# Kernel tuning notes

Measured on AMD Instinct MI355X. Metric: run time of the kernel, lower is better.

The kernel has to match this reference:

```python
import jax, jax.numpy as jnp
import numpy as np

N_NODES = 1536
IN_FEATURES = 1433
N_HIDDEN = 64      # total across 8 heads -> 8 per head
N_HEADS = 8
N_CLASSES = 7
NEG_SLOPE = 0.2    # LeakyReLU slope in GATv2 layer


def setup_inputs() -> dict:
    key = jax.random.key(0)
    k_x, k_adj, k_w1, k_a1, k_w2, k_a2 = jax.random.split(key, 6)
    x = jax.random.normal(k_x, (N_NODES, IN_FEATURES), dtype=jnp.float32)
    adj = jax.random.uniform(k_adj, (N_NODES, N_NODES)) < 0.01
    adj = adj | jnp.eye(N_NODES, dtype=bool)
    adj_mat = adj[:, :, None]  # [n, n, 1]
    # layer 1 (share_weights=True -> one linear for l and r), attn vector shared across heads
    s1 = 1.0 / np.sqrt(IN_FEATURES)
    W1 = jax.random.uniform(k_w1, (IN_FEATURES, N_HIDDEN), minval=-s1, maxval=s1, dtype=jnp.float32)
    a1 = jax.random.uniform(k_a1, (N_HIDDEN // N_HEADS,), minval=-1.0, maxval=1.0, dtype=jnp.float32)
    # layer 2: 1 head, n_classes features, is_concat=False (mean over the single head)
    s2 = 1.0 / np.sqrt(N_HIDDEN)
    W2 = jax.random.uniform(k_w2, (N_HIDDEN, N_CLASSES), minval=-s2, maxval=s2, dtype=jnp.float32)
    a2 = jax.random.uniform(k_a2, (N_CLASSES,), minval=-1.0, maxval=1.0, dtype=jnp.float32)
    return {"x": x, "adj_mat": adj_mat, "W1": W1, "a1": a1, "W2": W2, "a2": a2}


def _gatv2_layer(h, adj, W, a, n_heads, is_concat):
    n = h.shape[0]
    g = (h @ W).reshape(n, n_heads, -1)              # shared weights: g_l == g_r == g
    # pairwise scores: e[i,j,h] = a . leaky_relu(g[j] + g[i])  (symmetric since weights shared)
    s = jax.nn.leaky_relu(g[:, None] + g[None, :], NEG_SLOPE)   # [n, n, heads, f]
    e = jnp.einsum('ijhf,f->ijh', s, a)                          # [n, n, heads]
    e = jnp.where(adj, e, -jnp.inf)                              # adj broadcasts [n,n,1]
    att = jax.nn.softmax(e, axis=1)                              # softmax over source nodes j
    out = jnp.einsum('ijh,jhf->ihf', att, g)                     # [n, heads, f]
    if is_concat:
        return out.reshape(n, -1)
    return out.mean(axis=1)


def reference(x, adj_mat, W1, a1, W2, a2):
    # dropout layers are identity in eval mode
    h = _gatv2_layer(x, adj_mat, W1, a1, N_HEADS, True)   # [n, n_hidden]
    h = jax.nn.elu(h)
    return _gatv2_layer(h, adj_mat, W2, a2, 1, False)     # [n, n_classes]
```

## Files before the change

### kernel.cpp

```cpp
#include <hip/hip_runtime.h>

#define N_NODES 1536
#define IN_F    1433
#define HID     64
#define NH      8
#define HF      8
#define NC      7
#define MAXN    64
#define GST     66
#define G1_BLOCKS 384
#define ROWS    4
#define KQ      92
#define XS2     1472
#define RED_ST  260

__device__ __forceinline__ float waveAllMax(float v) {
#pragma unroll
    for (int o = 32; o > 0; o >>= 1) v = fmaxf(v, __shfl_xor(v, o, 64));
    return v;
}
__device__ __forceinline__ float waveAllSum(float v) {
#pragma unroll
    for (int o = 32; o > 0; o >>= 1) v += __shfl_xor(v, o, 64);
    return v;
}

__global__ __launch_bounds__(256) void k_front(const float* __restrict__ x,
                                               const float* __restrict__ W1,
                                               const unsigned int* __restrict__ adj,
                                               float* __restrict__ g1,
                                               int* __restrict__ cnt,
                                               int* __restrict__ nbr) {
    __shared__ float xs[ROWS * XS2];
    __shared__ float red[16 * RED_ST];
    __shared__ int lc;
    const int t = threadIdx.x;

    if (blockIdx.x < G1_BLOCKS) {
        const int i0 = blockIdx.x * ROWS;
        for (int r = 0; r < ROWS; ++r) {
            const float* xr = x + (size_t)(i0 + r) * IN_F;
            for (int k = t; k < XS2; k += 256)
                xs[r * XS2 + k] = (k < IN_F) ? xr[k] : 0.f;
        }
        __syncthreads();

        const int tc = t & 15;
        const int tq = t >> 4;
        const int k0 = tq * KQ;
        float acc[ROWS][4];
#pragma unroll
        for (int r = 0; r < ROWS; ++r)
#pragma unroll
            for (int cc = 0; cc < 4; ++cc) acc[r][cc] = 0.f;

        for (int kb = k0; kb < k0 + KQ; kb += 4) {
            float wv[4][4];
#pragma unroll
            for (int u = 0; u < 4; ++u) {
                int kc = kb + u;
                if (kc > IN_F - 1) kc = IN_F - 1;
                float4 wq = *(const float4*)(W1 + (size_t)kc * HID + tc * 4);
                wv[u][0] = wq.x; wv[u][1] = wq.y; wv[u][2] = wq.z; wv[u][3] = wq.w;
            }
#pragma unroll
            for (int r = 0; r < ROWS; ++r) {
                float4 xq = *(const float4*)(xs + r * XS2 + kb);
                float xr4[4] = {xq.x, xq.y, xq.z, xq.w};
#pragma unroll
                for (int u = 0; u < 4; ++u)
#pragma unroll
                    for (int cc = 0; cc < 4; ++cc)
                        acc[r][cc] += xr4[u] * wv[u][cc];
            }
        }
#pragma unroll
        for (int r = 0; r < ROWS; ++r)
#pragma unroll
            for (int cc = 0; cc < 4; ++cc)
                red[tq * RED_ST + r * 64 + tc * 4 + cc] = acc[r][cc];
        __syncthreads();
        float s = 0.f;
#pragma unroll
        for (int q = 0; q < 16; ++q) s += red[q * RED_ST + t];
        g1[(size_t)(i0 + (t >> 6)) * HID + (t & 63)] = s;
    } else {
        const int i = blockIdx.x - G1_BLOCKS;
        if (t == 0) lc = 0;
        __syncthreads();
        const unsigned int* row = adj + (size_t)i * N_NODES;
        for (int j = t; j < N_NODES; j += 256) {
            if (row[j] != 0u) {
                int p = atomicAdd(&lc, 1);
                if (p < MAXN) nbr[i * MAXN + p] = j;
            }
        }
        __syncthreads();
        if (t == 0) {
            int n = (lc > MAXN) ? MAXN : lc;
            if (n == 0) { nbr[i * MAXN] = i; n = 1; }
            cnt[i] = n;
        }
    }
}

__global__ __launch_bounds__(128) void k_attn1(const float* __restrict__ g1,
                                               const int* __restrict__ cnt,
                                               const int* __restrict__ nbr,
                                               const float* __restrict__ a1,
                                               const float* __restrict__ W2,
                                               float* __restrict__ g2) {
    __shared__ float gis[HID];
    __shared__ float gj[MAXN * GST];
    __shared__ float es[NH * GST];
    __shared__ float hrow[HID];
    const int i = blockIdx.x, tid = threadIdx.x;
    const int t = tid & 63, w = tid >> 6;
    const int n = cnt[i];

    if (tid < HID) gis[tid] = g1[(size_t)i * HID + tid];
    const int jn = nbr[i * MAXN + t];

    for (int l0 = 4 * w; l0 < n; l0 += 8) {
        float v[4];
#pragma unroll
        for (int u = 0; u < 4; ++u) {
            int l = l0 + u;
            int lc = (l < n) ? l : (n - 1);
            int j = __shfl(jn, lc, 64);
            v[u] = g1[(size_t)j * HID + t];
        }
#pragma unroll
        for (int u = 0; u < 4; ++u)
            if (l0 + u < n) gj[(l0 + u) * GST + t] = v[u];
    }
    __syncthreads();

    float av[HF];
#pragma unroll
    for (int f = 0; f < HF; ++f) av[f] = a1[f];

    float sc[4];
    if (t < n) {
#pragma unroll
        for (int hh = 0; hh < 4; ++hh) {
            const int h = 4 * w + hh;
            float s = 0.f;
#pragma unroll
            for (int f = 0; f < HF; ++f) {
                float v = gis[h * HF + f] + gj[t * GST + h * HF + f];
                v = (v >= 0.f) ? v : 0.2f * v;
                s += av[f] * v;
            }
            sc[hh] = s;
        }
    } else {
#pragma unroll
        for (int hh = 0; hh < 4; ++hh) sc[hh] = -INFINITY;
    }

#pragma unroll
    for (int hh = 0; hh < 4; ++hh) {
        const int h = 4 * w + hh;
        float m = waveAllMax(sc[hh]);
        float p = (t < n) ? __expf(sc[hh] - m) : 0.f;
        float S = waveAllSum(p);
        es[h * GST + t] = p / S;
    }

    const int c = 32 * w + (t & 31);
    const int h = c >> 3;
    float acc = 0.f;
    for (int l = (t >> 5); l < n; l += 2)
        acc += es[h * GST + l] * gj[l * GST + c];
    acc += __shfl_xor(acc, 32, 64);
    float hv = (acc > 0.f) ? acc : (__expf(acc) - 1.f);
    if (t < 32) hrow[c] = hv;
    __syncthreads();

    const float hvt = hrow[t];
#pragma unroll
    for (int cc = 0; cc < 4; ++cc) {
        const int cG = 4 * w + cc;
        if (cG < NC) {
            float v = hvt * W2[t * NC + cG];
            v = waveAllSum(v);
            if (t == 0) g2[(size_t)i * 8 + cG] = v;
        }
    }
}

__global__ __launch_bounds__(64) void k_back(const float* __restrict__ g2,
                                             const float* __restrict__ a2,
                                             const int* __restrict__ cnt,
                                             const int* __restrict__ nbr,
                                             float* __restrict__ out) {
    __shared__ float g2s[MAXN * 8];
    const int i = blockIdx.x, t = threadIdx.x;
    const int n = cnt[i];
    const int jn = nbr[i * MAXN + t];
    const int j = (t < n) ? jn : i;

    float4 lo = *(const float4*)(g2 + (size_t)j * 8);
    float4 hi = *(const float4*)(g2 + (size_t)j * 8 + 4);
    float4 slo = *(const float4*)(g2 + (size_t)i * 8);
    float4 shi = *(const float4*)(g2 + (size_t)i * 8 + 4);
    *(float4*)(g2s + t * 8) = lo;
    *(float4*)(g2s + t * 8 + 4) = hi;
    __syncthreads();

    const float self[NC] = {slo.x, slo.y, slo.z, slo.w, shi.x, shi.y, shi.z};

    float scv;
    if (t < n) {
        float s = 0.f;
#pragma unroll
        for (int c = 0; c < NC; ++c) {
            float v = self[c] + g2s[t * 8 + c];
            v = (v >= 0.f) ? v : 0.2f * v;
            s += a2[c] * v;
        }
        scv = s;
    } else scv = -INFINITY;

    float m = waveAllMax(scv);
    float p = (t < n) ? __expf(scv - m) : 0.f;
    float S = waveAllSum(p);

#pragma unroll
    for (int c = 0; c < NC; ++c) {
        float v = (t < n) ? p * g2s[t * 8 + c] : 0.f;
        float s = waveAllSum(v);
        if (t == c) out[(size_t)i * NC + c] = s / S;
    }
}

extern "C" void kernel_launch(void* const* d_in, const int* in_sizes, int n_in,
                              void* d_out, int out_size, void* d_ws, size_t ws_size,
                              hipStream_t stream) {
    (void)out_size; (void)ws_size;
    const void* px = nullptr; const void* padj = nullptr;
    const void* pW1 = nullptr; const void* pa1 = nullptr;
    const void* pW2 = nullptr; const void* pa2 = nullptr;
    for (int i = 0; i < n_in; ++i) {
        switch (in_sizes[i]) {
            case N_NODES * IN_F:    px   = d_in[i]; break;
            case N_NODES * N_NODES: padj = d_in[i]; break;
            case IN_F * HID:        pW1  = d_in[i]; break;
            case HF:                pa1  = d_in[i]; break;
            case HID * NC:          pW2  = d_in[i]; break;
            case NC:                pa2  = d_in[i]; break;
            default: break;
        }
    }
    if (!px && n_in > 0)   px   = d_in[0];
    if (!padj && n_in > 1) padj = d_in[1];
    if (!pW1 && n_in > 2)  pW1  = d_in[2];
    if (!pa1 && n_in > 3)  pa1  = d_in[3];
    if (!pW2 && n_in > 4)  pW2  = d_in[4];
    if (!pa2 && n_in > 5)  pa2  = d_in[5];

    char* w = (char*)d_ws;
    size_t off = 0;
    auto carve = [&](size_t bytes) -> char* {
        off = (off + 255) & ~(size_t)255;
        char* p = w + off; off += bytes; return p;
    };
    int*   cnt = (int*)  carve((size_t)N_NODES * 4);
    int*   nbr = (int*)  carve((size_t)N_NODES * MAXN * 4);
    float* g1  = (float*)carve((size_t)N_NODES * HID * 4);
    float* g2  = (float*)carve((size_t)N_NODES * 8 * 4);

    float* outp = (float*)d_out;

    k_front<<<G1_BLOCKS + N_NODES, 256, 0, stream>>>((const float*)px, (const float*)pW1,
                                                     (const unsigned int*)padj, g1, cnt, nbr);
    k_attn1<<<N_NODES, 128, 0, stream>>>(g1, cnt, nbr, (const float*)pa1,
                                         (const float*)pW2, g2);
    k_back<<<N_NODES, 64, 0, stream>>>(g2, (const float*)pa2, cnt, nbr, outp);
}
```

Measured before the change: 102.2 us.

## Fuse second-layer attention into first via per-node flags and spin-waits

Merges the layer-2 attention kernel into the layer-1 attention kernel. Each block publishes its g2 row and sets a release flag, then waits on its neighbors' flags before computing the output softmax. This removes a kernel launch and the g2 round trip between launches. In exchange it relies on all blocks being co-resident, risking deadlock or spin overhead. The neighbor gather is also unrolled to 8 rows per wave.

```diff
diff --git a/kernel.cpp b/kernel.cpp
--- a/kernel.cpp
+++ b/kernel.cpp
@@ -30,7 +30,8 @@
                                                const unsigned int* __restrict__ adj,
                                                float* __restrict__ g1,
                                                int* __restrict__ cnt,
-                                               int* __restrict__ nbr) {
+                                               int* __restrict__ nbr,
+                                               int* __restrict__ flag) {
     __shared__ float xs[ROWS * XS2];
     __shared__ float red[16 * RED_ST];
     __shared__ int lc;
@@ -86,7 +87,7 @@
         g1[(size_t)(i0 + (t >> 6)) * HID + (t & 63)] = s;
     } else {
         const int i = blockIdx.x - G1_BLOCKS;
-        if (t == 0) lc = 0;
+        if (t == 0) { lc = 0; flag[i] = 0; }
         __syncthreads();
         const unsigned int* row = adj + (size_t)i * N_NODES;
         for (int j = t; j < N_NODES; j += 256) {
@@ -104,16 +105,20 @@
     }
 }
 
-__global__ __launch_bounds__(128) void k_attn1(const float* __restrict__ g1,
-                                               const int* __restrict__ cnt,
-                                               const int* __restrict__ nbr,
-                                               const float* __restrict__ a1,
-                                               const float* __restrict__ W2,
-                                               float* __restrict__ g2) {
+__global__ __launch_bounds__(128, 3) void k_fused(const float* __restrict__ g1,
+                                                  const int* __restrict__ cnt,
+                                                  const int* __restrict__ nbr,
+                                                  const float* __restrict__ a1,
+                                                  const float* __restrict__ W2,
+                                                  const float* __restrict__ a2,
+                                                  float* __restrict__ g2,
+                                                  int* __restrict__ flag,
+                                                  float* __restrict__ out) {
     __shared__ float gis[HID];
     __shared__ float gj[MAXN * GST];
     __shared__ float es[NH * GST];
     __shared__ float hrow[HID];
+    __shared__ float g2self[8];
     const int i = blockIdx.x, tid = threadIdx.x;
     const int t = tid & 63, w = tid >> 6;
     const int n = cnt[i];
@@ -121,17 +126,17 @@
     if (tid < HID) gis[tid] = g1[(size_t)i * HID + tid];
     const int jn = nbr[i * MAXN + t];
 
-    for (int l0 = 4 * w; l0 < n; l0 += 8) {
-        float v[4];
-#pragma unroll
-        for (int u = 0; u < 4; ++u) {
+    for (int l0 = 8 * w; l0 < n; l0 += 16) {
+        float v[8];
+#pragma unroll
+        for (int u = 0; u < 8; ++u) {
             int l = l0 + u;
-            int lc = (l < n) ? l : (n - 1);
-            int j = __shfl(jn, lc, 64);
-            v[u] = g1[(size_t)j * HID + t];
-        }
-#pragma unroll
-        for (int u = 0; u < 4; ++u)
+            int lc2 = (l < n) ? l : (n - 1);
+            int j2 = __shfl(jn, lc2, 64);
+            v[u] = g1[(size_t)j2 * HID + t];
+        }
+#pragma unroll
+        for (int u = 0; u < 8; ++u)
             if (l0 + u < n) gj[(l0 + u) * GST + t] = v[u];
     }
     __syncthreads();
@@ -185,53 +190,48 @@
         if (cG < NC) {
             float v = hvt * W2[t * NC + cG];
             v = waveAllSum(v);
-            if (t == 0) g2[(size_t)i * 8 + cG] = v;
-        }
-    }
-}
-
-__global__ __launch_bounds__(64) void k_back(const float* __restrict__ g2,
-                                             const float* __restrict__ a2,
-                                             const int* __restrict__ cnt,
-                                             const int* __restrict__ nbr,
-                                             float* __restrict__ out) {
-    __shared__ float g2s[MAXN * 8];
-    const int i = blockIdx.x, t = threadIdx.x;
-    const int n = cnt[i];
-    const int jn = nbr[i * MAXN + t];
-    const int j = (t < n) ? jn : i;
-
-    float4 lo = *(const float4*)(g2 + (size_t)j * 8);
-    float4 hi = *(const float4*)(g2 + (size_t)j * 8 + 4);
-    float4 slo = *(const float4*)(g2 + (size_t)i * 8);
-    float4 shi = *(const float4*)(g2 + (size_t)i * 8 + 4);
-    *(float4*)(g2s + t * 8) = lo;
-    *(float4*)(g2s + t * 8 + 4) = hi;
+            if (t == 0) { g2[(size_t)i * 8 + cG] = v; g2self[cG] = v; }
+        }
+    }
+
     __syncthreads();
-
-    const float self[NC] = {slo.x, slo.y, slo.z, slo.w, shi.x, shi.y, shi.z};
-
-    float scv;
-    if (t < n) {
-        float s = 0.f;
-#pragma unroll
-        for (int c = 0; c < NC; ++c) {
-            float v = self[c] + g2s[t * 8 + c];
-            v = (v >= 0.f) ? v : 0.2f * v;
-            s += a2[c] * v;
-        }
-        scv = s;
-    } else scv = -INFINITY;
-
-    float m = waveAllMax(scv);
-    float p = (t < n) ? __expf(scv - m) : 0.f;
-    float S = waveAllSum(p);
-
-#pragma unroll
-    for (int c = 0; c < NC; ++c) {
-        float v = (t < n) ? p * g2s[t * 8 + c] : 0.f;
-        float s = waveAllSum(v);
-        if (t == c) out[(size_t)i * NC + c] = s / S;
+    if (tid == 0) {
+        __threadfence();
+        __hip_atomic_store(&flag[i], 1, __ATOMIC_RELEASE, __HIP_MEMORY_SCOPE_AGENT);
+    }
+
+    if (w == 0) {
+        const int j = (t < n) ? jn : i;
+        if (t < n) {
+            while (__hip_atomic_load(&flag[j], __ATOMIC_ACQUIRE,
+                                     __HIP_MEMORY_SCOPE_AGENT) == 0) {}
+        }
+        float4 lo = *(const float4*)(g2 + (size_t)j * 8);
+        float4 hi = *(const float4*)(g2 + (size_t)j * 8 + 4);
+        const float row[NC] = {lo.x, lo.y, lo.z, lo.w, hi.x, hi.y, hi.z};
+
+        float scv;
+        if (t < n) {
+            float s = 0.f;
+#pragma unroll
+            for (int cc2 = 0; cc2 < NC; ++cc2) {
+                float v = g2self[cc2] + row[cc2];
+                v = (v >= 0.f) ? v : 0.2f * v;
+                s += a2[cc2] * v;
+            }
+            scv = s;
+        } else scv = -INFINITY;
+
+        float m = waveAllMax(scv);
+        float p = (t < n) ? __expf(scv - m) : 0.f;
+        float S = waveAllSum(p);
+
+#pragma unroll
+        for (int cc2 = 0; cc2 < NC; ++cc2) {
+            float v = (t < n) ? p * row[cc2] : 0.f;
+            float s = waveAllSum(v);
+            if (t == cc2) out[(size_t)i * NC + cc2] = s / S;
+        }
     }
 }
 
@@ -266,16 +266,18 @@
         off = (off + 255) & ~(size_t)255;
         char* p = w + off; off += bytes; return p;
     };
-    int*   cnt = (int*)  carve((size_t)N_NODES * 4);
-    int*   nbr = (int*)  carve((size_t)N_NODES * MAXN * 4);
-    float* g1  = (float*)carve((size_t)N_NODES * HID * 4);
-    float* g2  = (float*)carve((size_t)N_NODES * 8 * 4);
+    int*   cnt  = (int*)  carve((size_t)N_NODES * 4);
+    int*   nbr  = (int*)  carve((size_t)N_NODES * MAXN * 4);
+    float* g1   = (float*)carve((size_t)N_NODES * HID * 4);
+    float* g2   = (float*)carve((size_t)N_NODES * 8 * 4);
+    int*   flag = (int*)  carve((size_t)N_NODES * 4);
 
     float* outp = (float*)d_out;
 
     k_front<<<G1_BLOCKS + N_NODES, 256, 0, stream>>>((const float*)px, (const float*)pW1,
-                                                     (const unsigned int*)padj, g1, cnt, nbr);
-    k_attn1<<<N_NODES, 128, 0, stream>>>(g1, cnt, nbr, (const float*)pa1,
-                                         (const float*)pW2, g2);
-    k_back<<<N_NODES, 64, 0, stream>>>(g2, (const float*)pa2, cnt, nbr, outp);
-}
+                                                     (const unsigned int*)padj, g1, cnt, nbr,
+                                                     flag);
+    k_fused<<<N_NODES, 128, 0, stream>>>(g1, cnt, nbr, (const float*)pa1,
+                                         (const float*)pW2, (const float*)pa2,
+                                         g2, flag, outp);
+}
```

New measurement: 181.3 us. 1.77x slower.
